# Kernel tuning notes

Measured on AMD Instinct MI355X. Metric: run time of the kernel, lower is better.

The kernel has to match this reference:

```python
import jax, jax.numpy as jnp
import numpy as np

B, S, F, DV, H, DH, L = 32, 600, 9, 1024, 16, 64, 2


def setup_inputs() -> dict:
    key = jax.random.key(0)
    ks = jax.random.split(key, 24)
    w = lambda k, shape, s=0.05: jax.random.normal(k, shape, dtype=jnp.float32) * s
    return {
        "x": w(ks[0], (B, S, F), 1.0),
        "enc_in_W": w(ks[1], (F, DV)), "enc_in_b": w(ks[2], (DV,)),
        "Wq": w(ks[3], (L, H, DV, DH)), "bq": w(ks[4], (L, H, DH)),
        "Wk": w(ks[5], (L, H, DV, DH)), "bk": w(ks[6], (L, H, DH)),
        "Wv": w(ks[7], (L, H, DV, DH)), "bv": w(ks[8], (L, H, DH)),
        "Wo": w(ks[9], (L, DV, DV)), "bo": w(ks[10], (L, DV)),
        "W1": w(ks[11], (L, DV, DV)), "b1": w(ks[12], (L, DV)),
        "W2": w(ks[13], (L, DV, DV)), "b2": w(ks[14], (L, DV)),
        "ln1_w": jnp.ones((L, DV)), "ln1_b": jnp.zeros((L, DV)),
        "ln2_w": jnp.ones((L, DV)), "ln2_b": jnp.zeros((L, DV)),
        "out_W": w(ks[15], (DV, F)), "out_b": w(ks[16], (F,)),
    }


def _layernorm(v, g, b):
    mu = v.mean(-1, keepdims=True)
    var = v.var(-1, keepdims=True)  # biased, matches torch LayerNorm
    return (v - mu) / jnp.sqrt(var + 1e-5) * g + b


def reference(x, enc_in_W, enc_in_b, Wq, bq, Wk, bk, Wv, bv, Wo, bo,
              W1, b1, W2, b2, ln1_w, ln1_b, ln2_w, ln2_b, out_W, out_b):
    # enc_input_fc; pe skipped (code checks pe_mode == 'stardard', never true)
    h = x @ enc_in_W + enc_in_b  # [B,S,DV]
    scale = 1.0 / jnp.sqrt(jnp.float32(DH))
    for l in range(L):
        q = jnp.einsum('bsd,hdk->bhsk', h, Wq[l]) + bq[l][None, :, None, :]
        k = jnp.einsum('bsd,hdk->bhsk', h, Wk[l]) + bk[l][None, :, None, :]
        v = jnp.einsum('bsd,hdk->bhsk', h, Wv[l]) + bv[l][None, :, None, :]
        attn = jax.nn.softmax(jnp.einsum('bhsk,bhtk->bhst', q, k) * scale, axis=-1)
        ctx = jnp.einsum('bhst,bhtk->bhsk', attn, v)  # [B,H,S,DH]
        # torch: stack(heads, dim=-1) -> [B,S,DH,H], then flatten(start_dim=2)
        a = ctx.transpose(0, 2, 3, 1).reshape(B, S, DH * H)
        attn_out = a @ Wo[l] + bo[l]
        x1 = _layernorm(h + attn_out, ln1_w[l], ln1_b[l])
        ff = jax.nn.elu(x1 @ W2[l] + b2[l]) @ W1[l] + b1[l]  # fc1(elu(fc2(x1)))
        h = _layernorm(x1 + ff, ln2_w[l], ln2_b[l])
    out = h @ out_W + out_b  # [B,S,F]; in_seq_len == out_seq_len -> no out_seq_fc
    return out
```

## Files before the change

kernel.cpp:

```cpp
#include <hip/hip_runtime.h>

typedef unsigned short u16;
typedef unsigned int u32;
typedef __attribute__((ext_vector_type(8))) short shortx8;
typedef __attribute__((ext_vector_type(4))) float floatx4;
typedef __attribute__((ext_vector_type(4))) u32 uintx4;

#define AS1 __attribute__((address_space(1)))
#define AS3 __attribute__((address_space(3)))

__device__ __forceinline__ float bf2f(u16 u) {
  return __builtin_bit_cast(float, ((u32)u) << 16);
}
__device__ __forceinline__ u16 f2bf(float f) {
  u32 i = __builtin_bit_cast(u32, f);
  u32 r = (i + 0x7fffu + ((i >> 16) & 1u)) >> 16;
  return (u16)r;
}

__launch_bounds__(256)
__global__ void pack_qkv(const float* __restrict__ Wq, const float* __restrict__ Wk,
                         const float* __restrict__ Wv, const float* __restrict__ bq,
                         const float* __restrict__ bk, const float* __restrict__ bv,
                         u16* __restrict__ Bt, float* __restrict__ bias) {
  const size_t i = (size_t)blockIdx.x * 256 + threadIdx.x;
  const int k = (int)(i & 1023);
  const size_t r = i >> 10;
  const int n = (int)(r % 3072);
  const int l = (int)(r / 3072);
  const int which = n >> 10;
  const int nn = n & 1023;
  const int hh = nn >> 6, dd = nn & 63;
  const float* src = (which == 0) ? Wq : (which == 1) ? Wk : Wv;
  const float* srcb = (which == 0) ? bq : (which == 1) ? bk : bv;
  float v = src[(((size_t)l * 16 + hh) * 1024 + k) * 64 + dd];
  Bt[i] = f2bf(v);
  if (k == 0) bias[(size_t)l * 3072 + n] = srcb[(size_t)l * 1024 + nn];
}

__launch_bounds__(256)
__global__ void pack_t(const float* __restrict__ W, u16* __restrict__ Bt) {
  const size_t i = (size_t)blockIdx.x * 256 + threadIdx.x;
  const int k = (int)(i & 1023);
  const size_t r = i >> 10;
  const int n = (int)(r & 1023);
  const int l = (int)(r >> 10);
  Bt[i] = f2bf(W[((size_t)l * 1024 + k) * 1024 + n]);
}

__launch_bounds__(256)
__global__ void enc_kernel(const float* __restrict__ x, const float* __restrict__ W,
                           const float* __restrict__ bias, u16* __restrict__ h) {
  const size_t i = (size_t)blockIdx.x * 256 + threadIdx.x;
  const int m = (int)(i >> 10), n = (int)(i & 1023);
  const float* xr = x + (size_t)m * 9;
  float acc = bias[n];
#pragma unroll
  for (int f = 0; f < 9; ++f) acc += xr[f] * W[f * 1024 + n];
  h[i] = f2bf(acc);
}

template <int EPI>
__launch_bounds__(256)
__global__ void gemm_bt(const u16* __restrict__ A, int lda,
                        const u16* __restrict__ Bt,
                        const float* __restrict__ bias,
                        const u16* __restrict__ R, int ldr,
                        u16* __restrict__ C, int ldc) {
  constexpr int K = 1024;
  __shared__ u16 As[128 * 64];
  __shared__ u16 Bs[128 * 64];
  const int tid = threadIdx.x;
  const int lane = tid & 63;
  const int w = tid >> 6;
  const int wr = w >> 1, wc = w & 1;
  const int m0 = blockIdx.y * 128, n0 = blockIdx.x * 128;

  floatx4 acc[4][4];
#pragma unroll
  for (int i = 0; i < 4; ++i)
#pragma unroll
    for (int j = 0; j < 4; ++j) acc[i][j] = (floatx4){0.f, 0.f, 0.f, 0.f};

  const u16* Ab = A + (size_t)m0 * lda;
  const u16* Bb = Bt + (size_t)n0 * K;

  for (int k0 = 0; k0 < K; k0 += 64) {
#pragma unroll
    for (int p = 0; p < 4; ++p) {
      const int o = p * 4096 + tid * 16;
      const int row = o >> 7;
      const int ke = (o & 127) >> 1;
      __builtin_amdgcn_global_load_lds((const AS1 void*)(Ab + (size_t)row * lda + (k0 + ke)),
                                       (AS3 void*)((char*)As + o), 16, 0, 0);
      __builtin_amdgcn_global_load_lds((const AS1 void*)(Bb + (size_t)row * K + (k0 + ke)),
                                       (AS3 void*)((char*)Bs + o), 16, 0, 0);
    }
    __syncthreads();
#pragma unroll
    for (int ks = 0; ks < 2; ++ks) {
      shortx8 af[4], bfr[4];
#pragma unroll
      for (int i = 0; i < 4; ++i) {
        const int ar = wr * 64 + i * 16 + (lane & 15);
        af[i] = *(const shortx8*)&As[ar * 64 + ks * 32 + (lane >> 4) * 8];
        const int br = wc * 64 + i * 16 + (lane & 15);
        bfr[i] = *(const shortx8*)&Bs[br * 64 + ks * 32 + (lane >> 4) * 8];
      }
#pragma unroll
      for (int i = 0; i < 4; ++i)
#pragma unroll
        for (int j = 0; j < 4; ++j)
          acc[i][j] = __builtin_amdgcn_mfma_f32_16x16x32_bf16(af[i], bfr[j], acc[i][j], 0, 0, 0);
    }
    __syncthreads();
  }

  const int lr = (lane >> 4) * 4, lc = lane & 15;
#pragma unroll
  for (int i = 0; i < 4; ++i) {
#pragma unroll
    for (int j = 0; j < 4; ++j) {
      const int col = n0 + wc * 64 + j * 16 + lc;
      const float bv = bias[col];
#pragma unroll
      for (int r = 0; r < 4; ++r) {
        const int row = m0 + wr * 64 + i * 16 + lr + r;
        float v = acc[i][j][r] + bv;
        if (EPI == 1) v += bf2f(R[(size_t)row * ldr + col]);
        if (EPI == 2) v = v > 0.f ? v : expm1f(v);
        C[(size_t)row * ldc + col] = f2bf(v);
      }
    }
  }
}

__launch_bounds__(256)
__global__ void attn_mfma(const u16* __restrict__ qkv, u16* __restrict__ aout) {
  const int qt = blockIdx.x, bh = blockIdx.y;
  const int b = bh >> 4, h = bh & 15;
  const int tid = threadIdx.x, lane = tid & 63, w = tid >> 6;
  const int g = lane >> 4, lq = lane & 15;

  __shared__ u16 K_ld[128 * 72];
  __shared__ u16 Vt[64 * 136];
  __shared__ u16 P_ld[4][16 * 136];

  const size_t bbase = (size_t)b * 600 * 3072;
  const int q0 = qt * 64 + w * 16;

  shortx8 aq[2];
  {
    const int s = q0 + lq;
    if (s < 600) {
      const u16* qp = qkv + bbase + (size_t)s * 3072 + h * 64 + g * 8;
      aq[0] = *(const shortx8*)qp;
      aq[1] = *(const shortx8*)(qp + 32);
    } else {
      aq[0] = (shortx8){0, 0, 0, 0, 0, 0, 0, 0};
      aq[1] = (shortx8){0, 0, 0, 0, 0, 0, 0, 0};
    }
  }

  floatx4 Oa[4];
#pragma unroll
  for (int db = 0; db < 4; ++db) Oa[db] = (floatx4){0.f, 0.f, 0.f, 0.f};
  float m[4], l[4];
#pragma unroll
  for (int r = 0; r < 4; ++r) { m[r] = -1e30f; l[r] = 0.f; }

  for (int ch = 0; ch < 5; ++ch) {
    const int t0 = ch * 128;
    __syncthreads();
    {
      const int tloc = tid >> 1, dhalf = (tid & 1) * 32;
      const int tg = t0 + tloc;
      if (tg < 600) {
        const u16* kp = qkv + bbase + (size_t)tg * 3072 + 1024 + h * 64 + dhalf;
        const u16* vp = kp + 1024;
#pragma unroll
        for (int c = 0; c < 4; ++c)
          *(uintx4*)&K_ld[tloc * 72 + dhalf + c * 8] = *(const uintx4*)(kp + c * 8);
#pragma unroll
        for (int c = 0; c < 4; ++c) {
          shortx8 vv = *(const shortx8*)(vp + c * 8);
#pragma unroll
          for (int e = 0; e < 8; ++e)
            Vt[(dhalf + c * 8 + e) * 136 + tloc] = (u16)vv[e];
        }
      } else {
        const uintx4 z4 = (uintx4){0, 0, 0, 0};
#pragma unroll
        for (int c = 0; c < 4; ++c)
          *(uintx4*)&K_ld[tloc * 72 + dhalf + c * 8] = z4;
#pragma unroll
        for (int c = 0; c < 4; ++c)
#pragma unroll
          for (int e = 0; e < 8; ++e)
            Vt[(dhalf + c * 8 + e) * 136 + tloc] = 0;
      }
    }
    __syncthreads();

    floatx4 S[8];
#pragma unroll
    for (int jb = 0; jb < 8; ++jb) {
      S[jb] = (floatx4){0.f, 0.f, 0.f, 0.f};
#pragma unroll
      for (int ks = 0; ks < 2; ++ks) {
        shortx8 bk = *(const shortx8*)&K_ld[(jb * 16 + lq) * 72 + ks * 32 + g * 8];
        S[jb] = __builtin_amdgcn_mfma_f32_16x16x32_bf16(aq[ks], bk, S[jb], 0, 0, 0);
      }
    }
#pragma unroll
    for (int jb = 0; jb < 8; ++jb) {
      const int tg = t0 + jb * 16 + lq;
      const bool ok = tg < 600;
#pragma unroll
      for (int r = 0; r < 4; ++r) S[jb][r] = ok ? S[jb][r] * 0.125f : -1e30f;
    }

    float scale[4];
#pragma unroll
    for (int r = 0; r < 4; ++r) {
      float v = S[0][r];
#pragma unroll
      for (int jb = 1; jb < 8; ++jb) v = fmaxf(v, S[jb][r]);
      v = fmaxf(v, __shfl_xor(v, 1));
      v = fmaxf(v, __shfl_xor(v, 2));
      v = fmaxf(v, __shfl_xor(v, 4));
      v = fmaxf(v, __shfl_xor(v, 8));
      const float mn = fmaxf(m[r], v);
      scale[r] = __expf(m[r] - mn);
      m[r] = mn;
      l[r] *= scale[r];
    }
#pragma unroll
    for (int db = 0; db < 4; ++db)
#pragma unroll
      for (int r = 0; r < 4; ++r) Oa[db][r] *= scale[r];

    float sums[4] = {0.f, 0.f, 0.f, 0.f};
#pragma unroll
    for (int jb = 0; jb < 8; ++jb)
#pragma unroll
      for (int r = 0; r < 4; ++r) {
        const float p = __expf(S[jb][r] - m[r]);
        sums[r] += p;
        P_ld[w][(g * 4 + r) * 136 + jb * 16 + lq] = f2bf(p);
      }
#pragma unroll
    for (int r = 0; r < 4; ++r) {
      float v = sums[r];
      v += __shfl_xor(v, 1);
      v += __shfl_xor(v, 2);
      v += __shfl_xor(v, 4);
      v += __shfl_xor(v, 8);
      l[r] += v;
    }

#pragma unroll
    for (int ks = 0; ks < 4; ++ks) {
      shortx8 ap = *(const shortx8*)&P_ld[w][lq * 136 + ks * 32 + g * 8];
#pragma unroll
      for (int db = 0; db < 4; ++db) {
        shortx8 bv = *(const shortx8*)&Vt[(db * 16 + lq) * 136 + ks * 32 + g * 8];
        Oa[db] = __builtin_amdgcn_mfma_f32_16x16x32_bf16(ap, bv, Oa[db], 0, 0, 0);
      }
    }
  }

#pragma unroll
  for (int r = 0; r < 4; ++r) {
    const int sg = q0 + g * 4 + r;
    if (sg < 600) {
      const float inv = 1.f / l[r];
      u16* orow = aout + ((size_t)(b * 600 + sg)) * 1024 + h;
#pragma unroll
      for (int db = 0; db < 4; ++db)
        orow[(size_t)(db * 16 + lq) * 16] = f2bf(Oa[db][r] * inv);
    }
  }
}

__launch_bounds__(256)
__global__ void ln_kernel(const u16* __restrict__ y, int ldy,
                          const float* __restrict__ g, const float* __restrict__ be,
                          u16* __restrict__ o, int ldo) {
  const int row = blockIdx.x, tid = threadIdx.x;
  const int lane = tid & 63, wv = tid >> 6;
  const u16* yr = y + (size_t)row * ldy;
  const int c = tid * 4;
  float v0 = bf2f(yr[c]), v1 = bf2f(yr[c + 1]);
  float v2 = bf2f(yr[c + 2]), v3 = bf2f(yr[c + 3]);
  float s = v0 + v1 + v2 + v3;
  float q = v0 * v0 + v1 * v1 + v2 * v2 + v3 * v3;
#pragma unroll
  for (int m = 32; m; m >>= 1) {
    s += __shfl_xor(s, m);
    q += __shfl_xor(q, m);
  }
  __shared__ float red[2][4];
  if (lane == 0) {
    red[0][wv] = s;
    red[1][wv] = q;
  }
  __syncthreads();
  s = red[0][0] + red[0][1] + red[0][2] + red[0][3];
  q = red[1][0] + red[1][1] + red[1][2] + red[1][3];
  const float mu = s * (1.f / 1024.f);
  const float var = q * (1.f / 1024.f) - mu * mu;
  const float rstd = rsqrtf(var + 1e-5f);
  u16* orow = o + (size_t)row * ldo;
  orow[c]     = f2bf((v0 - mu) * rstd * g[c] + be[c]);
  orow[c + 1] = f2bf((v1 - mu) * rstd * g[c + 1] + be[c + 1]);
  orow[c + 2] = f2bf((v2 - mu) * rstd * g[c + 2] + be[c + 2]);
  orow[c + 3] = f2bf((v3 - mu) * rstd * g[c + 3] + be[c + 3]);
}

__launch_bounds__(256)
__global__ void out_kernel(const u16* __restrict__ h, const float* __restrict__ W,
                           const float* __restrict__ bias, float* __restrict__ out) {
  const int m = blockIdx.x * 4 + (threadIdx.x >> 6);
  const int lane = threadIdx.x & 63;
  float acc[9];
#pragma unroll
  for (int f = 0; f < 9; ++f) acc[f] = 0.f;
  const u16* hr = h + (size_t)m * 1024;
#pragma unroll 4
  for (int j = 0; j < 16; ++j) {
    const int k = lane + j * 64;
    const float hv = bf2f(hr[k]);
    const float* wr = W + (size_t)k * 9;
#pragma unroll
    for (int f = 0; f < 9; ++f) acc[f] += hv * wr[f];
  }
#pragma unroll
  for (int f = 0; f < 9; ++f)
#pragma unroll
    for (int mm = 32; mm; mm >>= 1) acc[f] += __shfl_xor(acc[f], mm);
  if (lane < 9) out[(size_t)m * 9 + lane] = acc[lane] + bias[lane];
}

extern "C" void kernel_launch(void* const* d_in, const int* in_sizes, int n_in,
                              void* d_out, int out_size, void* d_ws, size_t ws_size,
                              hipStream_t stream) {
  (void)in_sizes; (void)n_in; (void)out_size; (void)ws_size;
  const float* x     = (const float*)d_in[0];
  const float* encW  = (const float*)d_in[1];
  const float* encB  = (const float*)d_in[2];
  const float* Wq    = (const float*)d_in[3];
  const float* bq    = (const float*)d_in[4];
  const float* Wk    = (const float*)d_in[5];
  const float* bk    = (const float*)d_in[6];
  const float* Wv    = (const float*)d_in[7];
  const float* bv    = (const float*)d_in[8];
  const float* Wo    = (const float*)d_in[9];
  const float* bo    = (const float*)d_in[10];
  const float* W1    = (const float*)d_in[11];
  const float* b1    = (const float*)d_in[12];
  const float* W2    = (const float*)d_in[13];
  const float* b2    = (const float*)d_in[14];
  const float* ln1w  = (const float*)d_in[15];
  const float* ln1b  = (const float*)d_in[16];
  const float* ln2w  = (const float*)d_in[17];
  const float* ln2b  = (const float*)d_in[18];
  const float* outW  = (const float*)d_in[19];
  const float* outB  = (const float*)d_in[20];
  float* out = (float*)d_out;

  char* ws = (char*)d_ws;
  size_t off = 0;
  auto alloc = [&](size_t bytes) -> void* {
    void* p = ws + off;
    off += (bytes + 255) & ~(size_t)255;
    return p;
  };
  u16* h    = (u16*)alloc(19660800ull * 2);
  u16* qkv  = (u16*)alloc(58982400ull * 2);
  u16* abuf = (u16*)alloc(19660800ull * 2);
  u16* Bqkv = (u16*)alloc(6291456ull * 2);
  u16* Bwo  = (u16*)alloc(2097152ull * 2);
  u16* Bw1  = (u16*)alloc(2097152ull * 2);
  u16* Bw2  = (u16*)alloc(2097152ull * 2);
  float* bqkv = (float*)alloc(6144ull * 4);
  u16* ybuf = qkv;
  u16* x1   = qkv + 1024;
  u16* mid  = qkv + 2048;
  u16* y2   = abuf;

  pack_qkv<<<24576, 256, 0, stream>>>(Wq, Wk, Wv, bq, bk, bv, Bqkv, bqkv);
  pack_t<<<8192, 256, 0, stream>>>(Wo, Bwo);
  pack_t<<<8192, 256, 0, stream>>>(W1, Bw1);
  pack_t<<<8192, 256, 0, stream>>>(W2, Bw2);
  enc_kernel<<<76800, 256, 0, stream>>>(x, encW, encB, h);

  for (int l = 0; l < 2; ++l) {
    gemm_bt<0><<<dim3(24, 150), 256, 0, stream>>>(
        h, 1024, Bqkv + (size_t)l * 3145728, bqkv + l * 3072, nullptr, 0, qkv, 3072);
    attn_mfma<<<dim3(10, 512), 256, 0, stream>>>(qkv, abuf);
    gemm_bt<1><<<dim3(8, 150), 256, 0, stream>>>(
        abuf, 1024, Bwo + (size_t)l * 1048576, bo + l * 1024, h, 1024, ybuf, 3072);
    ln_kernel<<<19200, 256, 0, stream>>>(ybuf, 3072, ln1w + l * 1024, ln1b + l * 1024, x1, 3072);
    gemm_bt<2><<<dim3(8, 150), 256, 0, stream>>>(
        x1, 3072, Bw2 + (size_t)l * 1048576, b2 + l * 1024, nullptr, 0, mid, 3072);
    gemm_bt<1><<<dim3(8, 150), 256, 0, stream>>>(
        mid, 3072, Bw1 + (size_t)l * 1048576, b1 + l * 1024, x1, 3072, y2, 1024);
    ln_kernel<<<19200, 256, 0, stream>>>(y2, 1024, ln2w + l * 1024, ln2b + l * 1024, h, 1024);
  }
  out_kernel<<<4800, 256, 0, stream>>>(h, outW, outB, out);
}
```

Baseline: 1.428 ms.

## Tile weight packing through LDS, stage GEMM epilogue for vectorized stores, vectorize layernorm

Weight packing kernels now transpose 64x64 tiles through shared memory with float4 reads and 16-byte writes, replacing strided scalar gathers. The GEMM epilogue writes results to a padded shared buffer, then does coalesced 16-byte stores with the residual add done in vector form. The layernorm kernel loads and stores with packed vectors. Risks: the residual is now added after bf16 rounding (double rounding), and the GEMM uses more LDS, which may limit occupancy.

New measurement: 1.458 ms. 2.1% more time.

```diff
diff --git a/kernel.cpp b/kernel.cpp
--- a/kernel.cpp
+++ b/kernel.cpp
@@ -5,6 +5,7 @@
 typedef __attribute__((ext_vector_type(8))) short shortx8;
 typedef __attribute__((ext_vector_type(4))) float floatx4;
 typedef __attribute__((ext_vector_type(4))) u32 uintx4;
+typedef __attribute__((ext_vector_type(2))) u32 uintx2;
 
 #define AS1 __attribute__((address_space(1)))
 #define AS3 __attribute__((address_space(3)))
@@ -19,33 +20,58 @@
 }
 
 __launch_bounds__(256)
-__global__ void pack_qkv(const float* __restrict__ Wq, const float* __restrict__ Wk,
-                         const float* __restrict__ Wv, const float* __restrict__ bq,
-                         const float* __restrict__ bk, const float* __restrict__ bv,
-                         u16* __restrict__ Bt, float* __restrict__ bias) {
-  const size_t i = (size_t)blockIdx.x * 256 + threadIdx.x;
-  const int k = (int)(i & 1023);
-  const size_t r = i >> 10;
-  const int n = (int)(r % 3072);
-  const int l = (int)(r / 3072);
-  const int which = n >> 10;
-  const int nn = n & 1023;
-  const int hh = nn >> 6, dd = nn & 63;
-  const float* src = (which == 0) ? Wq : (which == 1) ? Wk : Wv;
-  const float* srcb = (which == 0) ? bq : (which == 1) ? bk : bv;
-  float v = src[(((size_t)l * 16 + hh) * 1024 + k) * 64 + dd];
-  Bt[i] = f2bf(v);
-  if (k == 0) bias[(size_t)l * 3072 + n] = srcb[(size_t)l * 1024 + nn];
-}
-
-__launch_bounds__(256)
-__global__ void pack_t(const float* __restrict__ W, u16* __restrict__ Bt) {
-  const size_t i = (size_t)blockIdx.x * 256 + threadIdx.x;
-  const int k = (int)(i & 1023);
-  const size_t r = i >> 10;
-  const int n = (int)(r & 1023);
-  const int l = (int)(r >> 10);
-  Bt[i] = f2bf(W[((size_t)l * 1024 + k) * 1024 + n]);
+__global__ void pack_qkv_t(const float* __restrict__ W, u16* __restrict__ dst) {
+  __shared__ u16 T[64][72];
+  const int kt = blockIdx.x, y = blockIdx.y;
+  const int l = y >> 4, h = y & 15;
+  const int t = threadIdx.x;
+  const int rr = t >> 2, cq = (t & 3) * 16;
+  const float* src = W + ((size_t)y * 1024 + kt * 64 + rr) * 64 + cq;
+#pragma unroll
+  for (int e4 = 0; e4 < 4; ++e4) {
+    float4 f = *(const float4*)(src + e4 * 4);
+    T[cq + e4 * 4 + 0][rr] = f2bf(f.x);
+    T[cq + e4 * 4 + 1][rr] = f2bf(f.y);
+    T[cq + e4 * 4 + 2][rr] = f2bf(f.z);
+    T[cq + e4 * 4 + 3][rr] = f2bf(f.w);
+  }
+  __syncthreads();
+  const int dd = t >> 2, kq = (t & 3) * 16;
+  u16* drow = dst + (size_t)l * 3145728 + ((size_t)h * 64 + dd) * 1024 + kt * 64 + kq;
+  *(uintx4*)(drow) = *(const uintx4*)&T[dd][kq];
+  *(uintx4*)(drow + 8) = *(const uintx4*)&T[dd][kq + 8];
+}
+
+__launch_bounds__(256)
+__global__ void pack_sq_t(const float* __restrict__ W, u16* __restrict__ dst) {
+  __shared__ u16 T[64][72];
+  const int ct = blockIdx.x & 15, rt = blockIdx.x >> 4, l = blockIdx.y;
+  const int t = threadIdx.x;
+  const int rr = t >> 2, cq = (t & 3) * 16;
+  const float* src = W + (size_t)l * 1048576 + (size_t)(rt * 64 + rr) * 1024 + ct * 64 + cq;
+#pragma unroll
+  for (int e4 = 0; e4 < 4; ++e4) {
+    float4 f = *(const float4*)(src + e4 * 4);
+    T[cq + e4 * 4 + 0][rr] = f2bf(f.x);
+    T[cq + e4 * 4 + 1][rr] = f2bf(f.y);
+    T[cq + e4 * 4 + 2][rr] = f2bf(f.z);
+    T[cq + e4 * 4 + 3][rr] = f2bf(f.w);
+  }
+  __syncthreads();
+  const int cc = t >> 2, rq = (t & 3) * 16;
+  u16* drow = dst + (size_t)l * 1048576 + (size_t)(ct * 64 + cc) * 1024 + rt * 64 + rq;
+  *(uintx4*)(drow) = *(const uintx4*)&T[cc][rq];
+  *(uintx4*)(drow + 8) = *(const uintx4*)&T[cc][rq + 8];
+}
+
+__launch_bounds__(256)
+__global__ void pack_bias(const float* __restrict__ bq, const float* __restrict__ bk,
+                          const float* __restrict__ bv, float* __restrict__ bias) {
+  const int i = blockIdx.x * 256 + threadIdx.x;
+  const int l = i / 3072, n = i % 3072;
+  const int which = n >> 10, nn = n & 1023;
+  const float* s = (which == 0) ? bq : (which == 1) ? bk : bv;
+  bias[i] = s[l * 1024 + nn];
 }
 
 __launch_bounds__(256)
@@ -68,8 +94,9 @@
                         const u16* __restrict__ R, int ldr,
                         u16* __restrict__ C, int ldc) {
   constexpr int K = 1024;
-  __shared__ u16 As[128 * 64];
-  __shared__ u16 Bs[128 * 64];
+  __shared__ u16 sh[128 * 136];
+  u16* As = sh;
+  u16* Bs = sh + 8192;
   const int tid = threadIdx.x;
   const int lane = tid & 63;
   const int w = tid >> 6;
@@ -121,16 +148,43 @@
   for (int i = 0; i < 4; ++i) {
 #pragma unroll
     for (int j = 0; j < 4; ++j) {
-      const int col = n0 + wc * 64 + j * 16 + lc;
-      const float bv = bias[col];
+      const int col = wc * 64 + j * 16 + lc;
+      const float bv = bias[n0 + col];
 #pragma unroll
       for (int r = 0; r < 4; ++r) {
-        const int row = m0 + wr * 64 + i * 16 + lr + r;
+        const int row = wr * 64 + i * 16 + lr + r;
         float v = acc[i][j][r] + bv;
-        if (EPI == 1) v += bf2f(R[(size_t)row * ldr + col]);
         if (EPI == 2) v = v > 0.f ? v : expm1f(v);
-        C[(size_t)row * ldc + col] = f2bf(v);
-      }
+        sh[row * 136 + col] = f2bf(v);
+      }
+    }
+  }
+  __syncthreads();
+
+  {
+    const int row = tid >> 1, seg = (tid & 1) * 64;
+    u16* crow = C + (size_t)(m0 + row) * ldc + n0 + seg;
+    const u16* srow = sh + row * 136 + seg;
+    if (EPI == 1) {
+      const u16* rrow = R + (size_t)(m0 + row) * ldr + n0 + seg;
+#pragma unroll
+      for (int q = 0; q < 8; ++q) {
+        uintx4 cv = *(const uintx4*)(srow + q * 8);
+        uintx4 rv = *(const uintx4*)(rrow + q * 8);
+        uintx4 ov;
+#pragma unroll
+        for (int e = 0; e < 4; ++e) {
+          const u32 c2 = cv[e], r2 = rv[e];
+          const float lo = bf2f((u16)(c2 & 0xffffu)) + bf2f((u16)(r2 & 0xffffu));
+          const float hi = bf2f((u16)(c2 >> 16)) + bf2f((u16)(r2 >> 16));
+          ov[e] = (u32)f2bf(lo) | ((u32)f2bf(hi) << 16);
+        }
+        *(uintx4*)(crow + q * 8) = ov;
+      }
+    } else {
+#pragma unroll
+      for (int q = 0; q < 8; ++q)
+        *(uintx4*)(crow + q * 8) = *(const uintx4*)(srow + q * 8);
     }
   }
 }
@@ -291,8 +345,9 @@
   const int lane = tid & 63, wv = tid >> 6;
   const u16* yr = y + (size_t)row * ldy;
   const int c = tid * 4;
-  float v0 = bf2f(yr[c]), v1 = bf2f(yr[c + 1]);
-  float v2 = bf2f(yr[c + 2]), v3 = bf2f(yr[c + 3]);
+  const uintx2 yv = *(const uintx2*)&yr[c];
+  float v0 = bf2f((u16)(yv[0] & 0xffffu)), v1 = bf2f((u16)(yv[0] >> 16));
+  float v2 = bf2f((u16)(yv[1] & 0xffffu)), v3 = bf2f((u16)(yv[1] >> 16));
   float s = v0 + v1 + v2 + v3;
   float q = v0 * v0 + v1 * v1 + v2 * v2 + v3 * v3;
 #pragma unroll
@@ -311,11 +366,16 @@
   const float mu = s * (1.f / 1024.f);
   const float var = q * (1.f / 1024.f) - mu * mu;
   const float rstd = rsqrtf(var + 1e-5f);
-  u16* orow = o + (size_t)row * ldo;
-  orow[c]     = f2bf((v0 - mu) * rstd * g[c] + be[c]);
-  orow[c + 1] = f2bf((v1 - mu) * rstd * g[c + 1] + be[c + 1]);
-  orow[c + 2] = f2bf((v2 - mu) * rstd * g[c + 2] + be[c + 2]);
-  orow[c + 3] = f2bf((v3 - mu) * rstd * g[c + 3] + be[c + 3]);
+  const float4 gv = *(const float4*)&g[c];
+  const float4 bev = *(const float4*)&be[c];
+  const float o0 = (v0 - mu) * rstd * gv.x + bev.x;
+  const float o1 = (v1 - mu) * rstd * gv.y + bev.y;
+  const float o2 = (v2 - mu) * rstd * gv.z + bev.z;
+  const float o3 = (v3 - mu) * rstd * gv.w + bev.w;
+  uintx2 ov;
+  ov[0] = (u32)f2bf(o0) | ((u32)f2bf(o1) << 16);
+  ov[1] = (u32)f2bf(o2) | ((u32)f2bf(o3) << 16);
+  *(uintx2*)&o[(size_t)row * ldo + c] = ov;
 }
 
 __launch_bounds__(256)
@@ -389,10 +449,13 @@
   u16* mid  = qkv + 2048;
   u16* y2   = abuf;
 
-  pack_qkv<<<24576, 256, 0, stream>>>(Wq, Wk, Wv, bq, bk, bv, Bqkv, bqkv);
-  pack_t<<<8192, 256, 0, stream>>>(Wo, Bwo);
-  pack_t<<<8192, 256, 0, stream>>>(W1, Bw1);
-  pack_t<<<8192, 256, 0, stream>>>(W2, Bw2);
+  pack_qkv_t<<<dim3(16, 32), 256, 0, stream>>>(Wq, Bqkv);
+  pack_qkv_t<<<dim3(16, 32), 256, 0, stream>>>(Wk, Bqkv + 1048576);
+  pack_qkv_t<<<dim3(16, 32), 256, 0, stream>>>(Wv, Bqkv + 2097152);
+  pack_sq_t<<<dim3(256, 2), 256, 0, stream>>>(Wo, Bwo);
+  pack_sq_t<<<dim3(256, 2), 256, 0, stream>>>(W1, Bw1);
+  pack_sq_t<<<dim3(256, 2), 256, 0, stream>>>(W2, Bw2);
+  pack_bias<<<24, 256, 0, stream>>>(bq, bk, bv, bqkv);
   enc_kernel<<<76800, 256, 0, stream>>>(x, encW, encB, h);
 
   for (int l = 0; l < 2; ++l) {
```
